# Performance work log

Measured on AMD Instinct MI355X. Metric: run time of the kernel, lower is better.

## Reference

```python
import jax, jax.numpy as jnp
import numpy as np

B, T = 2, 512
D, H, DFF = 1024, 16, 4096
V, CSL = 32000, 16
NL, NDL = 4, 2
MAXLEN = 1024
DH = D // H


def generate_ar_mask(L, csl):
    m = np.zeros((2 * L, 2 * L), dtype=bool)
    for i in range(L):
        m[:i] = True
        m[L + (i // csl) * csl: L + i] = True
    return jnp.asarray(m)


def generate_block_ntp_mask(L, csl):
    m = np.zeros((2 * L, 2 * L), dtype=bool)
    for c in range(L // csl):
        if c - 1 >= 0:
            m[:(c - 1) * csl] = True
        m[L + c * csl: L + (c + 1) * csl] = True
    return jnp.asarray(m)


def layernorm(x, g, b, eps=1e-5):
    mu = x.mean(-1, keepdims=True)
    var = x.var(-1, keepdims=True)
    return (x - mu) / jnp.sqrt(var + eps) * g + b


def block(x, mask, p):
    ln1g, ln1b, wqkv, bqkv, wo, bo, ln2g, ln2b, w1, b1, w2, b2 = p
    h = layernorm(x, ln1g, ln1b)
    qkv = h @ wqkv + bqkv                       # [B,S,3D]
    q, k, v = jnp.split(qkv, 3, axis=-1)
    bs, S, _ = x.shape
    q = q.reshape(bs, S, H, DH).transpose(0, 2, 1, 3)
    k = k.reshape(bs, S, H, DH).transpose(0, 2, 1, 3)
    v = v.reshape(bs, S, H, DH).transpose(0, 2, 1, 3)
    scores = jnp.einsum('bhqd,bhkd->bhqk', q, k) / jnp.sqrt(jnp.asarray(DH, x.dtype))
    scores = jnp.where(mask, scores, jnp.asarray(-1e9, x.dtype))
    attn = jax.nn.softmax(scores, axis=-1)
    o = jnp.einsum('bhqk,bhkd->bhqd', attn, v)
    o = o.transpose(0, 2, 1, 3).reshape(bs, S, D)
    x = x + (o @ wo + bo)
    h = layernorm(x, ln2g, ln2b)
    return x + (jax.nn.gelu(h @ w1 + b1, approximate=False) @ w2 + b2)


def setup_inputs():
    key = jax.random.key(0)
    ks = jax.random.split(key, 6)

    def pstack(k, n):
        kk = jax.random.split(k, 4)
        return dict(
            ln1g=jnp.ones((n, D)), ln1b=jnp.zeros((n, D)),
            wqkv=0.02 * jax.random.normal(kk[0], (n, D, 3 * D)), bqkv=jnp.zeros((n, 3 * D)),
            wo=0.02 * jax.random.normal(kk[1], (n, D, D)), bo=jnp.zeros((n, D)),
            ln2g=jnp.ones((n, D)), ln2b=jnp.zeros((n, D)),
            w1=0.02 * jax.random.normal(kk[2], (n, D, DFF)), b1=jnp.zeros((n, DFF)),
            w2=0.02 * jax.random.normal(kk[3], (n, DFF, D)), b2=jnp.zeros((n, D)))

    body = pstack(ks[0], NL)
    dec = pstack(ks[1], NDL)
    inp = {
        'tok_ids': jax.random.randint(ks[2], (B, T), 0, V),
        'tok_emb': 0.02 * jax.random.normal(ks[3], (V, D)),
        'pos_emb': 0.02 * jax.random.normal(ks[4], (MAXLEN, D)),
        'mask_tokens': 0.02 * jax.random.normal(ks[5], (1, CSL, D)),
    }
    for kname, vv in body.items():
        inp['b_' + kname] = vv
    for kname, vv in dec.items():
        inp['d_' + kname] = vv
    return inp


def reference(tok_ids, tok_emb, pos_emb, mask_tokens,
              b_ln1g, b_ln1b, b_wqkv, b_bqkv, b_wo, b_bo, b_ln2g, b_ln2b, b_w1, b_b1, b_w2, b_b2,
              d_ln1g, d_ln1b, d_wqkv, d_bqkv, d_wo, d_bo, d_ln2g, d_ln2b, d_w1, d_b1, d_w2, d_b2):
    Bq, Tq = tok_ids.shape
    pos = jnp.tile(jnp.arange(Tq), 2)            # pos ids repeated for both halves
    emb_pos = pos_emb[pos]                       # [2T, D], broadcast over batch
    mask_ids = jnp.tile(mask_tokens, (Bq, Tq // CSL, 1))
    x = jnp.concatenate([tok_emb[tok_ids], mask_ids], axis=1) + emb_pos[None]

    body_mask = generate_block_ntp_mask(Tq, CSL)
    bp = (b_ln1g, b_ln1b, b_wqkv, b_bqkv, b_wo, b_bo, b_ln2g, b_ln2b, b_w1, b_b1, b_w2, b_b2)
    for i in range(NL):
        x = block(x, body_mask, tuple(p[i] for p in bp))

    ar_mask = generate_ar_mask(Tq, CSL)
    dp = (d_ln1g, d_ln1b, d_wqkv, d_bqkv, d_wo, d_bo, d_ln2g, d_ln2b, d_w1, d_b1, d_w2, d_b2)
    for i in range(NDL):
        x = block(x, ar_mask, tuple(p[i] for p in dp))

    logits = (x @ tok_emb.T)[:, Tq + 1:, :]      # [B, T-1, V]
    tgt = tok_ids[:, :-1].reshape(-1)
    logits = logits.reshape(-1, V)
    logp = jax.nn.log_softmax(logits, axis=-1)
    loss = -jnp.take_along_axis(logp, tgt[:, None], axis=1).mean()
    return loss
```

## Files before the change

### kernel.cpp

```cpp
#include <hip/hip_runtime.h>
#include <hip/hip_bf16.h>
#include <math.h>

#define DD   1024
#define HHN  16
#define DHD  64
#define DFFN 4096
#define VV   32000
#define BBN  2
#define TTN  512
#define SSN  1024
#define NRN  2048

typedef __attribute__((ext_vector_type(8))) short short8;
typedef __attribute__((ext_vector_type(4))) float f32x4;

enum : long {
    LSTR    = 12582912,
    OFF_QKV = 0,
    OFF_WO  = 3145728,
    OFF_W1  = 4194304,
    OFF_W2  = 8388608
};

struct P24 { const float* p[24]; };

__device__ __forceinline__ unsigned short f2bf(float f) {
    __hip_bfloat16 h = __float2bfloat16(f);
    return __builtin_bit_cast(unsigned short, h);
}
__device__ __forceinline__ float bf2f(unsigned short u) {
    return __bfloat162float(__builtin_bit_cast(__hip_bfloat16, u));
}

__device__ __forceinline__ void glds16(const void* g, void* l) {
    __builtin_amdgcn_global_load_lds(
        (const __attribute__((address_space(1))) void*)g,
        (__attribute__((address_space(3))) void*)l,
        16, 0, 0);
}

__device__ __forceinline__ float blockReduceSum(float v) {
    __shared__ float sh[4];
    #pragma unroll
    for (int o = 1; o < 64; o <<= 1) v += __shfl_xor(v, o, 64);
    int lane = threadIdx.x & 63, wv = threadIdx.x >> 6;
    __syncthreads();
    if (lane == 0) sh[wv] = v;
    __syncthreads();
    return sh[0] + sh[1] + sh[2] + sh[3];
}

__global__ __launch_bounds__(256) void prep_k(P24 wp, unsigned short* __restrict__ wbf,
                                              const int* __restrict__ tok,
                                              const float* __restrict__ temb,
                                              const float* __restrict__ pemb,
                                              const float* __restrict__ mtok,
                                              float* __restrict__ x) {
    __shared__ __align__(16) unsigned short Lb[128 * 72];
    const int id = blockIdx.x;
    const int t = threadIdx.x;

    if (id < 9216) {
        int seg, base, K, N;
        long woff;
        if (id < 2304)      { seg = 0; base = 0;    K = DD;   N = 3 * DD; woff = OFF_QKV; }
        else if (id < 3072) { seg = 1; base = 2304; K = DD;   N = DD;     woff = OFF_WO;  }
        else if (id < 6144) { seg = 2; base = 3072; K = DD;   N = DFFN;   woff = OFF_W1;  }
        else                { seg = 3; base = 6144; K = DFFN; N = DD;     woff = OFF_W2;  }
        const int rid = id - base;
        const int tpl = (K / 128) * (N / 64);
        const int lz = rid / tpl, t2 = rid % tpl;
        const int nt = N / 64;
        const int n0 = (t2 % nt) * 64, k0 = (t2 / nt) * 128;
        const float* w = wp.p[seg * 6 + lz];
        unsigned short* wt = wbf + (size_t)lz * LSTR + woff;

        const int kr = t >> 4;
        const int nc = (t & 15) * 4;
        #pragma unroll
        for (int p = 0; p < 8; p++) {
            const int k = p * 16 + kr;
            const int g = ((k >> 6) & 1) << 4;
            float4 f = *(const float4*)(w + (size_t)(k0 + k) * N + n0 + nc);
            __align__(8) unsigned short tmp[4];
            tmp[0] = f2bf(f.x); tmp[1] = f2bf(f.y);
            tmp[2] = f2bf(f.z); tmp[3] = f2bf(f.w);
            *(unsigned long long*)&Lb[k * 72 + (nc ^ g)] =
                *(const unsigned long long*)tmp;
        }
        __syncthreads();
        {
            const int rp  = t >> 3;
            const int sub = t & 7;
            const int kcg = sub >> 2;
            const int kh  = sub & 3;
            const int colx = (2 * rp) ^ (kcg << 4);
            const int kb = kcg * 64 + kh * 16;
            __align__(16) unsigned short tA[16], tB[16];
            #pragma unroll
            for (int i = 0; i < 16; i++) {
                unsigned int v = *(const unsigned int*)&Lb[(kb + i) * 72 + colx];
                tA[i] = (unsigned short)(v & 0xffff);
                tB[i] = (unsigned short)(v >> 16);
            }
            unsigned short* d0 = wt + (size_t)(n0 + 2 * rp) * K + k0 + kb;
            unsigned short* d1 = d0 + K;
            #pragma unroll
            for (int i = 0; i < 2; i++) {
                ((int4*)d0)[i] = ((const int4*)tA)[i];
                ((int4*)d1)[i] = ((const int4*)tB)[i];
            }
        }
    } else {
        const int row = id - 9216;
        const int b = row >> 10, s = row & 1023;
        const int d = t * 4;
        const float* src;
        const float* pe;
        if (s < TTN) {
            int tid2 = tok[b * TTN + s];
            src = temb + (size_t)tid2 * DD + d;
            pe  = pemb + (size_t)s * DD + d;
        } else {
            int sm = s - TTN;
            src = mtok + (size_t)(sm & 15) * DD + d;
            pe  = pemb + (size_t)sm * DD + d;
        }
        float4 v = *(const float4*)src;
        float4 p = *(const float4*)pe;
        v.x += p.x; v.y += p.y; v.z += p.z; v.w += p.w;
        *(float4*)(x + (size_t)row * DD + d) = v;
    }
}

__global__ __launch_bounds__(256) void ln_k(const float* __restrict__ x,
                                            const float* __restrict__ g,
                                            const float* __restrict__ b,
                                            unsigned short* __restrict__ out) {
    int row = blockIdx.x;
    int d = threadIdx.x * 4;
    const float4 v = *(const float4*)(x + (size_t)row * DD + d);
    float s  = v.x + v.y + v.z + v.w;
    float ss = v.x * v.x + v.y * v.y + v.z * v.z + v.w * v.w;
    s  = blockReduceSum(s);
    ss = blockReduceSum(ss);
    float mu  = s * (1.0f / DD);
    float var = ss * (1.0f / DD) - mu * mu;
    float inv = rsqrtf(var + 1e-5f);
    const float4 gg = *(const float4*)(g + d);
    const float4 bb = *(const float4*)(b + d);
    ushort4 o;
    o.x = f2bf((v.x - mu) * inv * gg.x + bb.x);
    o.y = f2bf((v.y - mu) * inv * gg.y + bb.y);
    o.z = f2bf((v.z - mu) * inv * gg.z + bb.z);
    o.w = f2bf((v.w - mu) * inv * gg.w + bb.w);
    *(ushort4*)(out + (size_t)row * DD + d) = o;
}

__global__ __launch_bounds__(256, 4) void flash_k(
    const unsigned short* __restrict__ qkvb,
    unsigned short* __restrict__ o,
    int mtype) {
    __shared__ __align__(16) unsigned short Qs[64][72];
    __shared__ __align__(16) unsigned short Ks[64][72];
    __shared__ __align__(16) unsigned short Vs[64][72];
    __shared__ __align__(16) unsigned short Ps[64][72];
    __shared__ float vcol[64];

    const int blk = blockIdx.x;
    const int bh = blk >> 4, qt = blk & 15;
    const int b = bh >> 4, h = bh & 15;
    const int t = threadIdx.x;
    const int lane = t & 63;
    const int w = t >> 6;
    const int fr = lane & 15;
    const int g8 = (lane >> 4) * 8;
    const int g4 = (lane >> 4) * 4;

    {
        const int r = t >> 2, c0 = (t & 3) * 16;
        const unsigned short* src =
            qkvb + (size_t)(b * SSN + qt * 64 + r) * 3072 + h * 64 + c0;
        *(int4*)&Qs[r][c0]     = *(const int4*)(src);
        *(int4*)&Qs[r][c0 + 8] = *(const int4*)(src + 8);
    }
    __syncthreads();
    short8 aq[2];
    #pragma unroll
    for (int kk = 0; kk < 2; kk++)
        aq[kk] = *(const short8*)&Qs[w * 16 + fr][kk * 32 + g8];

    float rsum[4] = {0.f, 0.f, 0.f, 0.f};
    f32x4 accO[4] = {};

    float vacc[16];
    #pragma unroll
    for (int j = 0; j < 16; j++) vacc[j] = 0.f;

    const unsigned short* kbase = qkvb + (size_t)(b * SSN) * 3072 + DD + h * 64;
    const unsigned short* vbase = qkvb + (size_t)(b * SSN) * 3072 + 2 * DD + h * 64;
    const int d0 = w * 16;

    for (int kt = 0; kt < 16; kt++) {
        __syncthreads();
        {
            const int r = t >> 2, c0 = (t & 3) * 16;
            const unsigned short* src = kbase + (size_t)(kt * 64 + r) * 3072 + c0;
            *(int4*)&Ks[r][c0]     = *(const int4*)(src);
            *(int4*)&Ks[r][c0 + 8] = *(const int4*)(src + 8);
        }
        {
            const unsigned short* src = vbase + (size_t)(kt * 64 + lane) * 3072 + d0;
            int4 q0 = *(const int4*)(src);
            int4 q1 = *(const int4*)(src + 8);
            const unsigned short* u = (const unsigned short*)&q0;
            #pragma unroll
            for (int j = 0; j < 8; j++) {
                Vs[d0 + j][lane] = u[j];
                vacc[j] += bf2f(u[j]);
            }
            const unsigned short* u2 = (const unsigned short*)&q1;
            #pragma unroll
            for (int j = 0; j < 8; j++) {
                Vs[d0 + 8 + j][lane] = u2[j];
                vacc[8 + j] += bf2f(u2[j]);
            }
        }
        __syncthreads();

        f32x4 a2[4] = {};
        #pragma unroll
        for (int n = 0; n < 4; n++) {
            short8 bk0 = *(const short8*)&Ks[n * 16 + fr][g8];
            short8 bk1 = *(const short8*)&Ks[n * 16 + fr][32 + g8];
            a2[n] = __builtin_amdgcn_mfma_f32_16x16x32_bf16(aq[0], bk0, a2[n], 0, 0, 0);
            a2[n] = __builtin_amdgcn_mfma_f32_16x16x32_bf16(aq[1], bk1, a2[n], 0, 0, 0);
        }
        #pragma unroll
        for (int j = 0; j < 4; j++) {
            #pragma unroll
            for (int n = 0; n < 4; n++) {
                float pv = __expf(a2[n][j] * 0.125f);
                rsum[j] += pv;
                Ps[w * 16 + g4 + j][n * 16 + fr] = f2bf(pv);
            }
        }
        #pragma unroll
        for (int kk = 0; kk < 2; kk++) {
            short8 pa = *(const short8*)&Ps[w * 16 + fr][kk * 32 + g8];
            #pragma unroll
            for (int nd = 0; nd < 4; nd++) {
                short8 vb = *(const short8*)&Vs[nd * 16 + fr][kk * 32 + g8];
                accO[nd] = __builtin_amdgcn_mfma_f32_16x16x32_bf16(pa, vb, accO[nd], 0, 0, 0);
            }
        }
    }

    float lrun[4];
    #pragma unroll
    for (int j = 0; j < 4; j++) {
        float rs = rsum[j];
        #pragma unroll
        for (int o2 = 1; o2 < 16; o2 <<= 1) rs += __shfl_xor(rs, o2, 64);
        lrun[j] = rs;
    }

    #pragma unroll
    for (int j = 0; j < 16; j++) {
        float vs = vacc[j];
        #pragma unroll
        for (int o2 = 1; o2 < 64; o2 <<= 1) vs += __shfl_xor(vs, o2, 64);
        if (lane == j) vcol[d0 + j] = vs;
    }
    __syncthreads();

    #pragma unroll
    for (int nd = 0; nd < 4; nd++)
        #pragma unroll
        for (int j = 0; j < 4; j++) {
            const int row = qt * 64 + w * 16 + g4 + j;
            const int col = nd * 16 + fr;
            bool uni;
            if (mtype == 0) uni = (row >= 480 && row < 512);
            else            uni = (row == 511) || (row >= 512 && (row & 15) == 15);
            float val;
            if (uni) val = vcol[col] * (1.0f / 1024.0f);
            else     val = accO[nd][j] / lrun[j];
            o[(size_t)(b * SSN + row) * DD + h * 64 + col] = f2bf(val);
        }
}

__global__ __launch_bounds__(256) void gxlconv_k(const float* __restrict__ x,
                                                 unsigned short* __restrict__ xl,
                                                 const float* __restrict__ temb,
                                                 unsigned short* __restrict__ tembb) {
    const int id = blockIdx.x;
    const int t = threadIdx.x;
    if (id < 1024) {
        int d = t * 4;
        ushort4 o = {0, 0, 0, 0};
        if (id < 1022) {
            int b = id / 511, i = id % 511;
            float4 v = *(const float4*)(x + (size_t)(b * SSN + 513 + i) * DD + d);
            o.x = f2bf(v.x); o.y = f2bf(v.y); o.z = f2bf(v.z); o.w = f2bf(v.w);
        }
        *(ushort4*)(xl + (size_t)id * DD + d) = o;
    } else {
        long i = ((long)(id - 1024) * 256 + t) * 8;
        float4 a = *(const float4*)(temb + i);
        float4 b = *(const float4*)(temb + i + 4);
        __align__(16) unsigned short tmp[8];
        tmp[0] = f2bf(a.x); tmp[1] = f2bf(a.y); tmp[2] = f2bf(a.z); tmp[3] = f2bf(a.w);
        tmp[4] = f2bf(b.x); tmp[5] = f2bf(b.y); tmp[6] = f2bf(b.z); tmp[7] = f2bf(b.w);
        *(int4*)(tembb + i) = *(const int4*)tmp;
    }
}

__global__ __launch_bounds__(256) void loss_row2_k(const float2* __restrict__ part,
                                                   const float* __restrict__ tgtlog,
                                                   float* __restrict__ rowloss) {
    const int r = blockIdx.x;
    const int t = threadIdx.x;
    float mx = -1e30f, s = 0.f;
    for (int i = t; i < 500; i += 256) {
        float2 p = part[(size_t)r * 500 + i];
        float m2 = fmaxf(mx, p.x);
        s = s * __expf(mx - m2) + p.y * __expf(p.x - m2);
        mx = m2;
    }
    #pragma unroll
    for (int o2 = 1; o2 < 64; o2 <<= 1) {
        float om = __shfl_xor(mx, o2, 64);
        float os = __shfl_xor(s, o2, 64);
        float m2 = fmaxf(mx, om);
        s = s * __expf(mx - m2) + os * __expf(om - m2);
        mx = m2;
    }
    __shared__ float shm[4], shs[4];
    int lane = t & 63, wv = t >> 6;
    if (lane == 0) { shm[wv] = mx; shs[wv] = s; }
    __syncthreads();
    if (t == 0) {
        float M = fmaxf(fmaxf(shm[0], shm[1]), fmaxf(shm[2], shm[3]));
        float S = shs[0] * __expf(shm[0] - M) + shs[1] * __expf(shm[1] - M)
                + shs[2] * __expf(shm[2] - M) + shs[3] * __expf(shm[3] - M);
        rowloss[r] = (logf(S) + M) - tgtlog[r];
    }
}

__global__ __launch_bounds__(256) void loss_final_k(const float* __restrict__ rowloss,
                                                    float* __restrict__ out) {
    int t = threadIdx.x;
    float s = 0.f;
    for (int i = t; i < 1022; i += 256) s += rowloss[i];
    s = blockReduceSum(s);
    if (t == 0) out[0] = s * (1.0f / 1022.0f);
}

template <int EPI, int KSPLIT, int BM>
__global__ __launch_bounds__(256) void gemm_k(
    const unsigned short* __restrict__ A, long lda,
    const unsigned short* __restrict__ Bt, long ldb,
    void* __restrict__ Cp, long ldc,
    const float* __restrict__ bias,
    int MT, int K, long kstr) {
    constexpr int MFRAG = BM / 32;
    __shared__ __align__(16) unsigned short As[2][BM][32];
    __shared__ __align__(16) unsigned short Bs[2][128][32];

    const int nwg = gridDim.x;
    const int q = nwg >> 3, r = nwg & 7;
    const int xcd = blockIdx.x & 7, lin = blockIdx.x >> 3;
    const int wg = (xcd < r ? xcd * (q + 1) : r * (q + 1) + (xcd - r) * q) + lin;
    const int tiles = nwg / KSPLIT;
    const int ks = wg / tiles;
    const int rem = wg % tiles;
    const int brow = (rem % MT) * BM;
    const int bcol = (rem / MT) * 128;
    const int Kl = K / KSPLIT;

    const int t = threadIdx.x;
    const int lane = t & 63;
    const int w = t >> 6;
    const int fr = lane & 15;
    const int g8 = (lane >> 4) * 8;

    const int sc = (lane & 3) * 8;
    const int srB = w * 32 + (lane >> 2);
    const unsigned short* bP0 = Bt + (size_t)(bcol + srB) * ldb + ks * Kl + sc;
    const unsigned short* bP1 = bP0 + (size_t)16 * ldb;
    const int srA = (BM == 128 ? w * 32 : w * 16) + (lane >> 2);
    const unsigned short* aP0 = A + (size_t)(brow + srA) * lda + ks * Kl + sc;
    const unsigned short* aP1 = aP0 + (size_t)16 * lda;

    f32x4 acc[MFRAG][4] = {};
    const int nsteps = Kl >> 5;

    auto stage = [&](int buf) {
        if constexpr (BM == 128) {
            glds16(aP0, &As[buf][w * 32][0]);
            glds16(aP1, &As[buf][w * 32 + 16][0]);
        } else {
            glds16(aP0, &As[buf][w * 16][0]);
        }
        glds16(bP0, &Bs[buf][w * 32][0]);
        glds16(bP1, &Bs[buf][w * 32 + 16][0]);
        aP0 += 32; aP1 += 32; bP0 += 32; bP1 += 32;
    };

    stage(0);
    asm volatile("s_waitcnt vmcnt(0)");
    __syncthreads();

    const int wrB = (w >> 1) * (BM / 2);
    int cur = 0;
    for (int s2 = 1; s2 < nsteps; ++s2) {
        const int nb = cur ^ 1;
        stage(nb);

        short8 af[MFRAG], bf[4];
        #pragma unroll
        for (int m = 0; m < MFRAG; m++)
            af[m] = *(const short8*)&As[cur][wrB + m * 16 + fr][g8];
        #pragma unroll
        for (int n = 0; n < 4; n++)
            bf[n] = *(const short8*)&Bs[cur][(w & 1) * 64 + n * 16 + fr][g8];
        #pragma unroll
        for (int m = 0; m < MFRAG; m++)
            #pragma unroll
            for (int n = 0; n < 4; n++)
                acc[m][n] = __builtin_amdgcn_mfma_f32_16x16x32_bf16(af[m], bf[n], acc[m][n], 0, 0, 0);
        __syncthreads();
        cur = nb;
    }
    {
        short8 af[MFRAG], bf[4];
        #pragma unroll
        for (int m = 0; m < MFRAG; m++)
            af[m] = *(const short8*)&As[cur][wrB + m * 16 + fr][g8];
        #pragma unroll
        for (int n = 0; n < 4; n++)
            bf[n] = *(const short8*)&Bs[cur][(w & 1) * 64 + n * 16 + fr][g8];
        #pragma unroll
        for (int m = 0; m < MFRAG; m++)
            #pragma unroll
            for (int n = 0; n < 4; n++)
                acc[m][n] = __builtin_amdgcn_mfma_f32_16x16x32_bf16(af[m], bf[n], acc[m][n], 0, 0, 0);
    }

    const int wc = (w & 1) * 64;
    const int g4 = (lane >> 4) * 4;
    #pragma unroll
    for (int n = 0; n < 4; n++) {
        const int col = bcol + wc + n * 16 + fr;
        const float bv = (bias && (KSPLIT == 1 || ks == 0)) ? bias[col] : 0.f;
        #pragma unroll
        for (int m = 0; m < MFRAG; m++) {
            #pragma unroll
            for (int j = 0; j < 4; j++) {
                const int row = brow + wrB + m * 16 + g4 + j;
                float v = acc[m][n][j] + bv;
                const size_t ci = (size_t)row * ldc + col;
                if (EPI == 0) {
                    ((float*)Cp)[ci] = v;
                } else if (EPI == 1) {
                    ((unsigned short*)Cp)[ci] = f2bf(v);
                } else if (EPI == 2) {
                    float gl = 0.5f * v * (1.0f + erff(v * 0.70710678118654752f));
                    ((unsigned short*)Cp)[ci] = f2bf(gl);
                } else if (EPI == 3) {
                    ((float*)Cp)[ci] += v;
                } else {
                    atomicAdd(&((float*)Cp)[ci], v);
                }
            }
        }
    }
}

__global__ __launch_bounds__(256) void gemm_lse_k(
    const unsigned short* __restrict__ A,
    const unsigned short* __restrict__ Bt,
    float2* __restrict__ part,
    float* __restrict__ tgtlog,
    const int* __restrict__ tok) {
    __shared__ __align__(16) unsigned short As[2][128][32];
    __shared__ __align__(16) unsigned short Bs[2][128][32];

    const int nwg = gridDim.x;
    const int q = nwg >> 3, r = nwg & 7;
    const int xcd = blockIdx.x & 7, lin = blockIdx.x >> 3;
    const int wg = (xcd < r ? xcd * (q + 1) : r * (q + 1) + (xcd - r) * q) + lin;
    const int MT = 8;
    const int brow = (wg % MT) * 128;
    const int bcol = (wg / MT) * 128;

    const int t = threadIdx.x;
    const int lane = t & 63;
    const int w = t >> 6;
    const int fr = lane & 15;
    const int g8 = (lane >> 4) * 8;

    const int sr = w * 32 + (lane >> 2);
    const int sc = (lane & 3) * 8;
    const unsigned short* aP0 = A + (size_t)(brow + sr) * DD + sc;
    const unsigned short* aP1 = aP0 + (size_t)16 * DD;
    const unsigned short* bP0 = Bt + (size_t)(bcol + sr) * DD + sc;
    const unsigned short* bP1 = bP0 + (size_t)16 * DD;

    f32x4 acc[4][4] = {};

    glds16(aP0, &As[0][w * 32][0]);
    glds16(aP1, &As[0][w * 32 + 16][0]);
    glds16(bP0, &Bs[0][w * 32][0]);
    glds16(bP1, &Bs[0][w * 32 + 16][0]);
    aP0 += 32; aP1 += 32; bP0 += 32; bP1 += 32;
    asm volatile("s_waitcnt vmcnt(0)");
    __syncthreads();

    int cur = 0;
    for (int s2 = 1; s2 < 32; ++s2) {
        const int nb = cur ^ 1;
        glds16(aP0, &As[nb][w * 32][0]);
        glds16(aP1, &As[nb][w * 32 + 16][0]);
        glds16(bP0, &Bs[nb][w * 32][0]);
        glds16(bP1, &Bs[nb][w * 32 + 16][0]);
        aP0 += 32; aP1 += 32; bP0 += 32; bP1 += 32;

        short8 af[4], bf[4];
        #pragma unroll
        for (int m = 0; m < 4; m++)
            af[m] = *(const short8*)&As[cur][(w >> 1) * 64 + m * 16 + fr][g8];
        #pragma unroll
        for (int n = 0; n < 4; n++)
            bf[n] = *(const short8*)&Bs[cur][(w & 1) * 64 + n * 16 + fr][g8];
        #pragma unroll
        for (int m = 0; m < 4; m++)
            #pragma unroll
            for (int n = 0; n < 4; n++)
                acc[m][n] = __builtin_amdgcn_mfma_f32_16x16x32_bf16(af[m], bf[n], acc[m][n], 0, 0, 0);
        __syncthreads();
        cur = nb;
    }
    {
        short8 af[4], bf[4];
        #pragma unroll
        for (int m = 0; m < 4; m++)
            af[m] = *(const short8*)&As[cur][(w >> 1) * 64 + m * 16 + fr][g8];
        #pragma unroll
        for (int n = 0; n < 4; n++)
            bf[n] = *(const short8*)&Bs[cur][(w & 1) * 64 + n * 16 + fr][g8];
        #pragma unroll
        for (int m = 0; m < 4; m++)
            #pragma unroll
            for (int n = 0; n < 4; n++)
                acc[m][n] = __builtin_amdgcn_mfma_f32_16x16x32_bf16(af[m], bf[n], acc[m][n], 0, 0, 0);
    }

    const int wr = (w >> 1) * 64;
    const int wc = (w & 1) * 64;
    const int g4 = (lane >> 4) * 4;
    const int ct2 = (bcol >> 7) * 2 + (w & 1);
    #pragma unroll
    for (int m = 0; m < 4; m++) {
        #pragma unroll
        for (int j = 0; j < 4; j++) {
            const int grow = brow + wr + m * 16 + g4 + j;
            const float v0 = acc[m][0][j], v1 = acc[m][1][j];
            const float v2 = acc[m][2][j], v3 = acc[m][3][j];
            float mx = fmaxf(fmaxf(v0, v1), fmaxf(v2, v3));
            #pragma unroll
            for (int o2 = 1; o2 < 16; o2 <<= 1) mx = fmaxf(mx, __shfl_xor(mx, o2, 64));
            float s = __expf(v0 - mx) + __expf(v1 - mx) + __expf(v2 - mx) + __expf(v3 - mx);
            #pragma unroll
            for (int o2 = 1; o2 < 16; o2 <<= 1) s += __shfl_xor(s, o2, 64);
            if (fr == 0) {
                float2 p; p.x = mx; p.y = s;
                part[(size_t)grow * 500 + ct2] = p;
            }
            int tgtc = -1;
            if (grow < 511) tgtc = tok[grow];
            else if (grow >= 511 && grow < 1022) tgtc = tok[512 + grow - 511];
            const int cl = tgtc - (bcol + wc);
            if (tgtc >= 0 && cl >= 0 && cl < 64 && (cl & 15) == fr) {
                const float vv[4] = {v0, v1, v2, v3};
                tgtlog[grow] = vv[cl >> 4];
            }
        }
    }
}

extern "C" void kernel_launch(void* const* d_in, const int* in_sizes, int n_in,
                              void* d_out, int out_size, void* d_ws, size_t ws_size,
                              hipStream_t stream) {
    const int*   tok  = (const int*)d_in[0];
    const float* temb = (const float*)d_in[1];
    const float* pemb = (const float*)d_in[2];
    const float* mtok = (const float*)d_in[3];
    const float* W[24];
    for (int i = 0; i < 24; i++) W[i] = (const float*)d_in[4 + i];

    char* ws = (char*)d_ws;
    float*          x      = (float*)(ws + 0);
    unsigned short* xb     = (unsigned short*)(ws + 8388608);
    unsigned short* qkvb   = (unsigned short*)(ws + 12582912);
    unsigned short* o      = (unsigned short*)(ws + 25165824);
    unsigned short* g      = (unsigned short*)(ws + 29360128);
    unsigned short* wbf    = (unsigned short*)(ws + 79691776);
    unsigned short* tembb  = (unsigned short*)(ws + 79691776);
    float2*         part   = (float2*)(ws + 145227776);
    float*          tgtlog = (float*)(ws + 149327872);
    unsigned short* xl     = (unsigned short*)(ws + 230686720);
    float*          rowloss= (float*)(ws + 232783872);

    P24 wp;
    for (int l = 0; l < 6; l++) {
        const int grp = (l < 4) ? 0 : 1;
        const int li  = (l < 4) ? l : l - 4;
        const float* const* P = W + grp * 12;
        wp.p[0 + l]  = P[2]  + (size_t)li * DD * 3 * DD;
        wp.p[6 + l]  = P[4]  + (size_t)li * DD * DD;
        wp.p[12 + l] = P[8]  + (size_t)li * DD * DFFN;
        wp.p[18 + l] = P[10] + (size_t)li * DFFN * DD;
    }
    prep_k<<<9216 + 2048, 256, 0, stream>>>(wp, wbf, tok, temb, pemb, mtok, x);

    for (int l = 0; l < 6; l++) {
        const int grp = (l < 4) ? 0 : 1;
        const int li  = (l < 4) ? l : l - 4;
        const float* const* P = W + grp * 12;
        const float* ln1g = P[0] + (size_t)li * DD;
        const float* ln1b = P[1] + (size_t)li * DD;
        const float* bqkv = P[3] + (size_t)li * 3 * DD;
        const float* bo   = P[5] + (size_t)li * DD;
        const float* ln2g = P[6] + (size_t)li * DD;
        const float* ln2b = P[7] + (size_t)li * DD;
        const float* b1   = P[9] + (size_t)li * DFFN;
        const float* b2   = P[11] + (size_t)li * DD;
        unsigned short* wl = wbf + (size_t)l * LSTR;

        if (l == 0) ln_k<<<NRN, 256, 0, stream>>>(x, ln1g, ln1b, xb);
        gemm_k<1, 1, 64><<<32 * 24, 256, 0, stream>>>(xb, DD, wl + OFF_QKV, DD,
                                                      qkvb, 3 * DD, bqkv, 32, DD, 0);
        flash_k<<<512, 256, 0, stream>>>(qkvb, o, grp);
        gemm_k<3, 1, 64><<<32 * 8, 256, 0, stream>>>(o, DD, wl + OFF_WO, DD,
                                                     x, DD, bo, 32, DD, 0);

        ln_k<<<NRN, 256, 0, stream>>>(x, ln2g, ln2b, xb);
        gemm_k<2, 1, 128><<<16 * 32, 256, 0, stream>>>(xb, DD, wl + OFF_W1, DD,
                                                       g, DFFN, b1, 16, DD, 0);
        gemm_k<4, 4, 128><<<16 * 8 * 4, 256, 0, stream>>>(g, DFFN, wl + OFF_W2, DFFN,
                                                          x, DD, b2, 16, DFFN, 0);
        if (l < 5) {
            const int l2 = l + 1;
            const int grp2 = (l2 < 4) ? 0 : 1;
            const int li2  = (l2 < 4) ? l2 : l2 - 4;
            const float* const* P2 = W + grp2 * 12;
            ln_k<<<NRN, 256, 0, stream>>>(x, P2[0] + (size_t)li2 * DD,
                                          P2[1] + (size_t)li2 * DD, xb);
        } else {
            gxlconv_k<<<1024 + 16000, 256, 0, stream>>>(x, xl, temb, tembb);
        }
    }

    gemm_lse_k<<<2000, 256, 0, stream>>>(xl, tembb, part, tgtlog, tok);
    loss_row2_k<<<1022, 256, 0, stream>>>(part, tgtlog, rowloss);
    loss_final_k<<<1, 256, 0, stream>>>(rowloss, (float*)d_out);
}
```

Measured before the change: 1.404 ms.

## Fuse all transformer layers into persistent megakernel with grid barriers

Replaces the per-layer chain of LN, GEMM and flash-attention launches with one persistent kernel of 512 blocks. The blocks step through every stage and synchronise with a software grid barrier built on atomics. The tok_emb bf16 conversion moves into the prep kernel, and the final loss reduction is folded into the row kernel with an atomic add. This removes about 40 launches and their tail gaps. In exchange, every stage now runs with fixed tile shapes, and correctness depends on all 512 blocks being co-resident (launch bounds of 2 blocks per CU); otherwise the barrier can deadlock.

```diff
diff --git a/kernel.cpp b/kernel.cpp
--- a/kernel.cpp
+++ b/kernel.cpp
@@ -24,6 +24,10 @@
 };
 
 struct P24 { const float* p[24]; };
+struct MegaP {
+    const float *ln1g[6], *ln1b[6], *bqkv[6], *bo[6];
+    const float *ln2g[6], *ln2b[6], *b1[6], *b2[6];
+};
 
 __device__ __forceinline__ unsigned short f2bf(float f) {
     __hip_bfloat16 h = __float2bfloat16(f);
@@ -40,15 +44,18 @@
         16, 0, 0);
 }
 
-__device__ __forceinline__ float blockReduceSum(float v) {
-    __shared__ float sh[4];
-    #pragma unroll
-    for (int o = 1; o < 64; o <<= 1) v += __shfl_xor(v, o, 64);
-    int lane = threadIdx.x & 63, wv = threadIdx.x >> 6;
-    __syncthreads();
-    if (lane == 0) sh[wv] = v;
-    __syncthreads();
-    return sh[0] + sh[1] + sh[2] + sh[3];
+__device__ __forceinline__ void gbar(unsigned* bar, unsigned nb) {
+    __syncthreads();
+    if (threadIdx.x == 0) {
+        __threadfence();
+        unsigned old = __hip_atomic_fetch_add(bar, 1u, __ATOMIC_RELEASE,
+                                              __HIP_MEMORY_SCOPE_AGENT);
+        const unsigned need = (old / nb + 1u) * nb;
+        while (__hip_atomic_load(bar, __ATOMIC_ACQUIRE,
+                                 __HIP_MEMORY_SCOPE_AGENT) < need)
+            __builtin_amdgcn_s_sleep(8);
+    }
+    __syncthreads();
 }
 
 __global__ __launch_bounds__(256) void prep_k(P24 wp, unsigned short* __restrict__ wbf,
@@ -56,7 +63,8 @@
                                               const float* __restrict__ temb,
                                               const float* __restrict__ pemb,
                                               const float* __restrict__ mtok,
-                                              float* __restrict__ x) {
+                                              float* __restrict__ x,
+                                              unsigned short* __restrict__ tembb) {
     __shared__ __align__(16) unsigned short Lb[128 * 72];
     const int id = blockIdx.x;
     const int t = threadIdx.x;
@@ -112,7 +120,7 @@
                 ((int4*)d1)[i] = ((const int4*)tB)[i];
             }
         }
-    } else {
+    } else if (id < 11264) {
         const int row = id - 9216;
         const int b = row >> 10, s = row & 1023;
         const int d = t * 4;
@@ -131,43 +139,169 @@
         float4 p = *(const float4*)pe;
         v.x += p.x; v.y += p.y; v.z += p.z; v.w += p.w;
         *(float4*)(x + (size_t)row * DD + d) = v;
-    }
-}
-
-__global__ __launch_bounds__(256) void ln_k(const float* __restrict__ x,
+    } else {
+        long i = ((long)(id - 11264) * 256 + t) * 8;
+        float4 a = *(const float4*)(temb + i);
+        float4 b = *(const float4*)(temb + i + 4);
+        __align__(16) unsigned short tmp[8];
+        tmp[0] = f2bf(a.x); tmp[1] = f2bf(a.y); tmp[2] = f2bf(a.z); tmp[3] = f2bf(a.w);
+        tmp[4] = f2bf(b.x); tmp[5] = f2bf(b.y); tmp[6] = f2bf(b.z); tmp[7] = f2bf(b.w);
+        *(int4*)(tembb + i) = *(const int4*)tmp;
+    }
+}
+
+
+__device__ __forceinline__ void dev_ln_wave(const float* __restrict__ x,
                                             const float* __restrict__ g,
                                             const float* __restrict__ b,
-                                            unsigned short* __restrict__ out) {
-    int row = blockIdx.x;
-    int d = threadIdx.x * 4;
-    const float4 v = *(const float4*)(x + (size_t)row * DD + d);
-    float s  = v.x + v.y + v.z + v.w;
-    float ss = v.x * v.x + v.y * v.y + v.z * v.z + v.w * v.w;
-    s  = blockReduceSum(s);
-    ss = blockReduceSum(ss);
-    float mu  = s * (1.0f / DD);
-    float var = ss * (1.0f / DD) - mu * mu;
-    float inv = rsqrtf(var + 1e-5f);
-    const float4 gg = *(const float4*)(g + d);
-    const float4 bb = *(const float4*)(b + d);
-    ushort4 o;
-    o.x = f2bf((v.x - mu) * inv * gg.x + bb.x);
-    o.y = f2bf((v.y - mu) * inv * gg.y + bb.y);
-    o.z = f2bf((v.z - mu) * inv * gg.z + bb.z);
-    o.w = f2bf((v.w - mu) * inv * gg.w + bb.w);
-    *(ushort4*)(out + (size_t)row * DD + d) = o;
-}
-
-__global__ __launch_bounds__(256, 4) void flash_k(
-    const unsigned short* __restrict__ qkvb,
-    unsigned short* __restrict__ o,
-    int mtype) {
-    __shared__ __align__(16) unsigned short Qs[64][72];
-    __shared__ __align__(16) unsigned short Ks[64][72];
-    __shared__ __align__(16) unsigned short Vs[64][72];
-    __shared__ __align__(16) unsigned short Ps[64][72];
-    __shared__ float vcol[64];
-
+                                            unsigned short* __restrict__ out, int row) {
+    const int lane = threadIdx.x & 63;
+    float4 v[4];
+    float s = 0.f, ss = 0.f;
+    #pragma unroll
+    for (int c = 0; c < 4; c++) {
+        v[c] = *(const float4*)(x + (size_t)row * DD + c * 256 + lane * 4);
+        s  += v[c].x + v[c].y + v[c].z + v[c].w;
+        ss += v[c].x * v[c].x + v[c].y * v[c].y + v[c].z * v[c].z + v[c].w * v[c].w;
+    }
+    #pragma unroll
+    for (int o2 = 1; o2 < 64; o2 <<= 1) {
+        s  += __shfl_xor(s, o2, 64);
+        ss += __shfl_xor(ss, o2, 64);
+    }
+    const float mu  = s * (1.0f / DD);
+    const float var = ss * (1.0f / DD) - mu * mu;
+    const float inv = rsqrtf(var + 1e-5f);
+    #pragma unroll
+    for (int c = 0; c < 4; c++) {
+        const int d = c * 256 + lane * 4;
+        const float4 gg = *(const float4*)(g + d);
+        const float4 bb = *(const float4*)(b + d);
+        ushort4 ov;
+        ov.x = f2bf((v[c].x - mu) * inv * gg.x + bb.x);
+        ov.y = f2bf((v[c].y - mu) * inv * gg.y + bb.y);
+        ov.z = f2bf((v[c].z - mu) * inv * gg.z + bb.z);
+        ov.w = f2bf((v[c].w - mu) * inv * gg.w + bb.w);
+        *(ushort4*)(out + (size_t)row * DD + d) = ov;
+    }
+}
+
+template <int EPI, int BM>
+__device__ __forceinline__ void dev_gemm(
+    unsigned short* LDSU,
+    int brow, int bcol, long kOff, int Kl, bool addBias,
+    const unsigned short* __restrict__ A, long lda,
+    const unsigned short* __restrict__ Bt, long ldb,
+    void* __restrict__ Cp, long ldc,
+    const float* __restrict__ bias) {
+    constexpr int MFRAG = BM / 32;
+    unsigned short* AsB = LDSU;
+    unsigned short* BsB = LDSU + 2 * BM * 32;
+
+    const int t = threadIdx.x;
+    const int lane = t & 63;
+    const int w = t >> 6;
+    const int fr = lane & 15;
+    const int g8 = (lane >> 4) * 8;
+
+    const int sc = (lane & 3) * 8;
+    const int srB = w * 32 + (lane >> 2);
+    const unsigned short* bP0 = Bt + (size_t)(bcol + srB) * ldb + kOff + sc;
+    const unsigned short* bP1 = bP0 + (size_t)16 * ldb;
+    const int srA = (BM == 128 ? w * 32 : w * 16) + (lane >> 2);
+    const unsigned short* aP0 = A + (size_t)(brow + srA) * lda + kOff + sc;
+    const unsigned short* aP1 = aP0 + (size_t)16 * lda;
+
+    f32x4 acc[MFRAG][4] = {};
+    const int nsteps = Kl >> 5;
+
+    auto stage = [&](int buf) {
+        unsigned short* ab = AsB + buf * (BM * 32);
+        unsigned short* bb = BsB + buf * (128 * 32);
+        if constexpr (BM == 128) {
+            glds16(aP0, ab + (w * 32) * 32);
+            glds16(aP1, ab + (w * 32 + 16) * 32);
+        } else {
+            glds16(aP0, ab + (w * 16) * 32);
+        }
+        glds16(bP0, bb + (w * 32) * 32);
+        glds16(bP1, bb + (w * 32 + 16) * 32);
+        aP0 += 32; aP1 += 32; bP0 += 32; bP1 += 32;
+    };
+
+    stage(0);
+    asm volatile("s_waitcnt vmcnt(0)");
+    __syncthreads();
+
+    const int wrB = (w >> 1) * (BM / 2);
+    int cur = 0;
+    for (int s2 = 1; s2 < nsteps; ++s2) {
+        const int nb = cur ^ 1;
+        stage(nb);
+
+        short8 af[MFRAG], bf[4];
+        #pragma unroll
+        for (int m = 0; m < MFRAG; m++)
+            af[m] = *(const short8*)(AsB + cur * (BM * 32) + (wrB + m * 16 + fr) * 32 + g8);
+        #pragma unroll
+        for (int n = 0; n < 4; n++)
+            bf[n] = *(const short8*)(BsB + cur * (128 * 32) + ((w & 1) * 64 + n * 16 + fr) * 32 + g8);
+        #pragma unroll
+        for (int m = 0; m < MFRAG; m++)
+            #pragma unroll
+            for (int n = 0; n < 4; n++)
+                acc[m][n] = __builtin_amdgcn_mfma_f32_16x16x32_bf16(af[m], bf[n], acc[m][n], 0, 0, 0);
+        __syncthreads();
+        cur = nb;
+    }
+    {
+        short8 af[MFRAG], bf[4];
+        #pragma unroll
+        for (int m = 0; m < MFRAG; m++)
+            af[m] = *(const short8*)(AsB + cur * (BM * 32) + (wrB + m * 16 + fr) * 32 + g8);
+        #pragma unroll
+        for (int n = 0; n < 4; n++)
+            bf[n] = *(const short8*)(BsB + cur * (128 * 32) + ((w & 1) * 64 + n * 16 + fr) * 32 + g8);
+        #pragma unroll
+        for (int m = 0; m < MFRAG; m++)
+            #pragma unroll
+            for (int n = 0; n < 4; n++)
+                acc[m][n] = __builtin_amdgcn_mfma_f32_16x16x32_bf16(af[m], bf[n], acc[m][n], 0, 0, 0);
+    }
+    __syncthreads();
+
+    const int wc = (w & 1) * 64;
+    const int g4 = (lane >> 4) * 4;
+    #pragma unroll
+    for (int n = 0; n < 4; n++) {
+        const int col = bcol + wc + n * 16 + fr;
+        const float bv = (bias && addBias) ? bias[col] : 0.f;
+        #pragma unroll
+        for (int m = 0; m < MFRAG; m++) {
+            #pragma unroll
+            for (int j = 0; j < 4; j++) {
+                const int row = brow + wrB + m * 16 + g4 + j;
+                float v = acc[m][n][j] + bv;
+                const size_t ci = (size_t)row * ldc + col;
+                if (EPI == 1) {
+                    ((unsigned short*)Cp)[ci] = f2bf(v);
+                } else if (EPI == 2) {
+                    float gl = 0.5f * v * (1.0f + erff(v * 0.70710678118654752f));
+                    ((unsigned short*)Cp)[ci] = f2bf(gl);
+                } else if (EPI == 3) {
+                    ((float*)Cp)[ci] += v;
+                } else {
+                    atomicAdd(&((float*)Cp)[ci], v);
+                }
+            }
+        }
+    }
+}
+
+__device__ __forceinline__ void dev_flash(unsigned short* Lf,
+                                          const unsigned short* __restrict__ qkvb,
+                                          unsigned short* __restrict__ o, int mtype) {
+    float* vcol = (float*)(Lf + 18432);
     const int blk = blockIdx.x;
     const int bh = blk >> 4, qt = blk & 15;
     const int b = bh >> 4, h = bh & 15;
@@ -182,18 +316,17 @@
         const int r = t >> 2, c0 = (t & 3) * 16;
         const unsigned short* src =
             qkvb + (size_t)(b * SSN + qt * 64 + r) * 3072 + h * 64 + c0;
-        *(int4*)&Qs[r][c0]     = *(const int4*)(src);
-        *(int4*)&Qs[r][c0 + 8] = *(const int4*)(src + 8);
+        *(int4*)&Lf[r * 72 + c0]     = *(const int4*)(src);
+        *(int4*)&Lf[r * 72 + c0 + 8] = *(const int4*)(src + 8);
     }
     __syncthreads();
     short8 aq[2];
     #pragma unroll
     for (int kk = 0; kk < 2; kk++)
-        aq[kk] = *(const short8*)&Qs[w * 16 + fr][kk * 32 + g8];
+        aq[kk] = *(const short8*)&Lf[(w * 16 + fr) * 72 + kk * 32 + g8];
 
     float rsum[4] = {0.f, 0.f, 0.f, 0.f};
     f32x4 accO[4] = {};
-
     float vacc[16];
     #pragma unroll
     for (int j = 0; j < 16; j++) vacc[j] = 0.f;
@@ -207,8 +340,8 @@
         {
             const int r = t >> 2, c0 = (t & 3) * 16;
             const unsigned short* src = kbase + (size_t)(kt * 64 + r) * 3072 + c0;
-            *(int4*)&Ks[r][c0]     = *(const int4*)(src);
-            *(int4*)&Ks[r][c0 + 8] = *(const int4*)(src + 8);
+            *(int4*)&Lf[4608 + r * 72 + c0]     = *(const int4*)(src);
+            *(int4*)&Lf[4608 + r * 72 + c0 + 8] = *(const int4*)(src + 8);
         }
         {
             const unsigned short* src = vbase + (size_t)(kt * 64 + lane) * 3072 + d0;
@@ -217,13 +350,13 @@
             const unsigned short* u = (const unsigned short*)&q0;
             #pragma unroll
             for (int j = 0; j < 8; j++) {
-                Vs[d0 + j][lane] = u[j];
+                Lf[9216 + (d0 + j) * 72 + lane] = u[j];
                 vacc[j] += bf2f(u[j]);
             }
             const unsigned short* u2 = (const unsigned short*)&q1;
             #pragma unroll
             for (int j = 0; j < 8; j++) {
-                Vs[d0 + 8 + j][lane] = u2[j];
+                Lf[9216 + (d0 + 8 + j) * 72 + lane] = u2[j];
                 vacc[8 + j] += bf2f(u2[j]);
             }
         }
@@ -232,8 +365,8 @@
         f32x4 a2[4] = {};
         #pragma unroll
         for (int n = 0; n < 4; n++) {
-            short8 bk0 = *(const short8*)&Ks[n * 16 + fr][g8];
-            short8 bk1 = *(const short8*)&Ks[n * 16 + fr][32 + g8];
+            short8 bk0 = *(const short8*)&Lf[4608 + (n * 16 + fr) * 72 + g8];
+            short8 bk1 = *(const short8*)&Lf[4608 + (n * 16 + fr) * 72 + 32 + g8];
             a2[n] = __builtin_amdgcn_mfma_f32_16x16x32_bf16(aq[0], bk0, a2[n], 0, 0, 0);
             a2[n] = __builtin_amdgcn_mfma_f32_16x16x32_bf16(aq[1], bk1, a2[n], 0, 0, 0);
         }
@@ -243,15 +376,15 @@
             for (int n = 0; n < 4; n++) {
                 float pv = __expf(a2[n][j] * 0.125f);
                 rsum[j] += pv;
-                Ps[w * 16 + g4 + j][n * 16 + fr] = f2bf(pv);
+                Lf[13824 + (w * 16 + g4 + j) * 72 + n * 16 + fr] = f2bf(pv);
             }
         }
         #pragma unroll
         for (int kk = 0; kk < 2; kk++) {
-            short8 pa = *(const short8*)&Ps[w * 16 + fr][kk * 32 + g8];
+            short8 pa = *(const short8*)&Lf[13824 + (w * 16 + fr) * 72 + kk * 32 + g8];
             #pragma unroll
             for (int nd = 0; nd < 4; nd++) {
-                short8 vb = *(const short8*)&Vs[nd * 16 + fr][kk * 32 + g8];
+                short8 vb = *(const short8*)&Lf[9216 + (nd * 16 + fr) * 72 + kk * 32 + g8];
                 accO[nd] = __builtin_amdgcn_mfma_f32_16x16x32_bf16(pa, vb, accO[nd], 0, 0, 0);
             }
         }
@@ -265,7 +398,6 @@
         for (int o2 = 1; o2 < 16; o2 <<= 1) rs += __shfl_xor(rs, o2, 64);
         lrun[j] = rs;
     }
-
     #pragma unroll
     for (int j = 0; j < 16; j++) {
         float vs = vacc[j];
@@ -289,37 +421,191 @@
             else     val = accO[nd][j] / lrun[j];
             o[(size_t)(b * SSN + row) * DD + h * 64 + col] = f2bf(val);
         }
-}
-
-__global__ __launch_bounds__(256) void gxlconv_k(const float* __restrict__ x,
-                                                 unsigned short* __restrict__ xl,
-                                                 const float* __restrict__ temb,
-                                                 unsigned short* __restrict__ tembb) {
-    const int id = blockIdx.x;
+    __syncthreads();
+}
+
+__device__ __forceinline__ void dev_gxl(const float* __restrict__ x,
+                                        unsigned short* __restrict__ xl, int r) {
+    const int d = threadIdx.x * 4;
+    ushort4 ov = {0, 0, 0, 0};
+    if (r < 1022) {
+        int b = r / 511, i = r % 511;
+        float4 v = *(const float4*)(x + (size_t)(b * SSN + 513 + i) * DD + d);
+        ov.x = f2bf(v.x); ov.y = f2bf(v.y); ov.z = f2bf(v.z); ov.w = f2bf(v.w);
+    }
+    if (r < 1024) *(ushort4*)(xl + (size_t)r * DD + d) = ov;
+}
+
+__global__ __launch_bounds__(256, 2) void mega_k(
+    MegaP P, const unsigned short* __restrict__ wbf,
+    float* __restrict__ x, unsigned short* __restrict__ xb,
+    unsigned short* __restrict__ qkvb, unsigned short* __restrict__ o,
+    unsigned short* __restrict__ g, unsigned short* __restrict__ xl,
+    unsigned* bar) {
+    __shared__ __align__(16) unsigned short LDSU[18560];
+    const int blk = blockIdx.x;
+    const unsigned NB = gridDim.x;
+
+    dev_ln_wave(x, P.ln1g[0], P.ln1b[0], xb, blk * 4 + (threadIdx.x >> 6));
+    gbar(bar, NB);
+
+    for (int l = 0; l < 6; ++l) {
+        const unsigned short* wl = wbf + (size_t)l * LSTR;
+
+        for (int tt = blk; tt < 384; tt += NB)
+            dev_gemm<1, 128>(LDSU, (tt & 15) * 128, (tt >> 4) * 128, 0, DD, true,
+                             xb, DD, wl + OFF_QKV, DD, qkvb, 3 * DD, P.bqkv[l]);
+        gbar(bar, NB);
+
+        dev_flash(LDSU, qkvb, o, (l < 4) ? 0 : 1);
+        gbar(bar, NB);
+
+        for (int tt = blk; tt < 256; tt += NB)
+            dev_gemm<3, 64>(LDSU, (tt & 31) * 64, (tt >> 5) * 128, 0, DD, true,
+                            o, DD, wl + OFF_WO, DD, x, DD, P.bo[l]);
+        gbar(bar, NB);
+
+        dev_ln_wave(x, P.ln2g[l], P.ln2b[l], xb, blk * 4 + (threadIdx.x >> 6));
+        gbar(bar, NB);
+
+        for (int tt = blk; tt < 512; tt += NB)
+            dev_gemm<2, 128>(LDSU, (tt & 15) * 128, (tt >> 4) * 128, 0, DD, true,
+                             xb, DD, wl + OFF_W1, DD, g, DFFN, P.b1[l]);
+        gbar(bar, NB);
+
+        for (int tt = blk; tt < 512; tt += NB) {
+            const int rem = tt & 127, ks = tt >> 7;
+            dev_gemm<4, 128>(LDSU, (rem & 15) * 128, (rem >> 4) * 128,
+                             (long)ks * 1024, 1024, ks == 0,
+                             g, DFFN, wl + OFF_W2, DFFN, x, DD, P.b2[l]);
+        }
+        gbar(bar, NB);
+
+        if (l < 5) {
+            dev_ln_wave(x, P.ln1g[l + 1], P.ln1b[l + 1], xb, blk * 4 + (threadIdx.x >> 6));
+            gbar(bar, NB);
+        } else {
+            dev_gxl(x, xl, blk * 2);
+            dev_gxl(x, xl, blk * 2 + 1);
+        }
+    }
+}
+
+__global__ __launch_bounds__(256) void gemm_lse_k(
+    const unsigned short* __restrict__ A,
+    const unsigned short* __restrict__ Bt,
+    float2* __restrict__ part,
+    float* __restrict__ tgtlog,
+    const int* __restrict__ tok) {
+    __shared__ __align__(16) unsigned short As[2][128][32];
+    __shared__ __align__(16) unsigned short Bs[2][128][32];
+
+    const int nwg = gridDim.x;
+    const int q = nwg >> 3, r = nwg & 7;
+    const int xcd = blockIdx.x & 7, lin = blockIdx.x >> 3;
+    const int wg = (xcd < r ? xcd * (q + 1) : r * (q + 1) + (xcd - r) * q) + lin;
+    const int MT = 8;
+    const int brow = (wg % MT) * 128;
+    const int bcol = (wg / MT) * 128;
+
     const int t = threadIdx.x;
-    if (id < 1024) {
-        int d = t * 4;
-        ushort4 o = {0, 0, 0, 0};
-        if (id < 1022) {
-            int b = id / 511, i = id % 511;
-            float4 v = *(const float4*)(x + (size_t)(b * SSN + 513 + i) * DD + d);
-            o.x = f2bf(v.x); o.y = f2bf(v.y); o.z = f2bf(v.z); o.w = f2bf(v.w);
-        }
-        *(ushort4*)(xl + (size_t)id * DD + d) = o;
-    } else {
-        long i = ((long)(id - 1024) * 256 + t) * 8;
-        float4 a = *(const float4*)(temb + i);
-        float4 b = *(const float4*)(temb + i + 4);
-        __align__(16) unsigned short tmp[8];
-        tmp[0] = f2bf(a.x); tmp[1] = f2bf(a.y); tmp[2] = f2bf(a.z); tmp[3] = f2bf(a.w);
-        tmp[4] = f2bf(b.x); tmp[5] = f2bf(b.y); tmp[6] = f2bf(b.z); tmp[7] = f2bf(b.w);
-        *(int4*)(tembb + i) = *(const int4*)tmp;
+    const int lane = t & 63;
+    const int w = t >> 6;
+    const int fr = lane & 15;
+    const int g8 = (lane >> 4) * 8;
+
+    const int sr = w * 32 + (lane >> 2);
+    const int sc = (lane & 3) * 8;
+    const unsigned short* aP0 = A + (size_t)(brow + sr) * DD + sc;
+    const unsigned short* aP1 = aP0 + (size_t)16 * DD;
+    const unsigned short* bP0 = Bt + (size_t)(bcol + sr) * DD + sc;
+    const unsigned short* bP1 = bP0 + (size_t)16 * DD;
+
+    f32x4 acc[4][4] = {};
+
+    glds16(aP0, &As[0][w * 32][0]);
+    glds16(aP1, &As[0][w * 32 + 16][0]);
+    glds16(bP0, &Bs[0][w * 32][0]);
+    glds16(bP1, &Bs[0][w * 32 + 16][0]);
+    aP0 += 32; aP1 += 32; bP0 += 32; bP1 += 32;
+    asm volatile("s_waitcnt vmcnt(0)");
+    __syncthreads();
+
+    int cur = 0;
+    for (int s2 = 1; s2 < 32; ++s2) {
+        const int nb = cur ^ 1;
+        glds16(aP0, &As[nb][w * 32][0]);
+        glds16(aP1, &As[nb][w * 32 + 16][0]);
+        glds16(bP0, &Bs[nb][w * 32][0]);
+        glds16(bP1, &Bs[nb][w * 32 + 16][0]);
+        aP0 += 32; aP1 += 32; bP0 += 32; bP1 += 32;
+
+        short8 af[4], bf[4];
+        #pragma unroll
+        for (int m = 0; m < 4; m++)
+            af[m] = *(const short8*)&As[cur][(w >> 1) * 64 + m * 16 + fr][g8];
+        #pragma unroll
+        for (int n = 0; n < 4; n++)
+            bf[n] = *(const short8*)&Bs[cur][(w & 1) * 64 + n * 16 + fr][g8];
+        #pragma unroll
+        for (int m = 0; m < 4; m++)
+            #pragma unroll
+            for (int n = 0; n < 4; n++)
+                acc[m][n] = __builtin_amdgcn_mfma_f32_16x16x32_bf16(af[m], bf[n], acc[m][n], 0, 0, 0);
+        __syncthreads();
+        cur = nb;
+    }
+    {
+        short8 af[4], bf[4];
+        #pragma unroll
+        for (int m = 0; m < 4; m++)
+            af[m] = *(const short8*)&As[cur][(w >> 1) * 64 + m * 16 + fr][g8];
+        #pragma unroll
+        for (int n = 0; n < 4; n++)
+            bf[n] = *(const short8*)&Bs[cur][(w & 1) * 64 + n * 16 + fr][g8];
+        #pragma unroll
+        for (int m = 0; m < 4; m++)
+            #pragma unroll
+            for (int n = 0; n < 4; n++)
+                acc[m][n] = __builtin_amdgcn_mfma_f32_16x16x32_bf16(af[m], bf[n], acc[m][n], 0, 0, 0);
+    }
+
+    const int wr = (w >> 1) * 64;
+    const int wc = (w & 1) * 64;
+    const int g4 = (lane >> 4) * 4;
+    const int ct2 = (bcol >> 7) * 2 + (w & 1);
+    #pragma unroll
+    for (int m = 0; m < 4; m++) {
+        #pragma unroll
+        for (int j = 0; j < 4; j++) {
+            const int grow = brow + wr + m * 16 + g4 + j;
+            const float v0 = acc[m][0][j], v1 = acc[m][1][j];
+            const float v2 = acc[m][2][j], v3 = acc[m][3][j];
+            float mx = fmaxf(fmaxf(v0, v1), fmaxf(v2, v3));
+            #pragma unroll
+            for (int o2 = 1; o2 < 16; o2 <<= 1) mx = fmaxf(mx, __shfl_xor(mx, o2, 64));
+            float s = __expf(v0 - mx) + __expf(v1 - mx) + __expf(v2 - mx) + __expf(v3 - mx);
+            #pragma unroll
+            for (int o2 = 1; o2 < 16; o2 <<= 1) s += __shfl_xor(s, o2, 64);
+            if (fr == 0) {
+                float2 p; p.x = mx; p.y = s;
+                part[(size_t)grow * 500 + ct2] = p;
+            }
+            int tgtc = -1;
+            if (grow < 511) tgtc = tok[grow];
+            else if (grow >= 511 && grow < 1022) tgtc = tok[512 + grow - 511];
+            const int cl = tgtc - (bcol + wc);
+            if (tgtc >= 0 && cl >= 0 && cl < 64 && (cl & 15) == fr) {
+                const float vv[4] = {v0, v1, v2, v3};
+                tgtlog[grow] = vv[cl >> 4];
+            }
+        }
     }
 }
 
 __global__ __launch_bounds__(256) void loss_row2_k(const float2* __restrict__ part,
                                                    const float* __restrict__ tgtlog,
-                                                   float* __restrict__ rowloss) {
+                                                   float* __restrict__ out) {
     const int r = blockIdx.x;
     const int t = threadIdx.x;
     float mx = -1e30f, s = 0.f;
@@ -345,249 +631,7 @@
         float M = fmaxf(fmaxf(shm[0], shm[1]), fmaxf(shm[2], shm[3]));
         float S = shs[0] * __expf(shm[0] - M) + shs[1] * __expf(shm[1] - M)
                 + shs[2] * __expf(shm[2] - M) + shs[3] * __expf(shm[3] - M);
-        rowloss[r] = (logf(S) + M) - tgtlog[r];
-    }
-}
-
-__global__ __launch_bounds__(256) void loss_final_k(const float* __restrict__ rowloss,
-                                                    float* __restrict__ out) {
-    int t = threadIdx.x;
-    float s = 0.f;
-    for (int i = t; i < 1022; i += 256) s += rowloss[i];
-    s = blockReduceSum(s);
-    if (t == 0) out[0] = s * (1.0f / 1022.0f);
-}
-
-template <int EPI, int KSPLIT, int BM>
-__global__ __launch_bounds__(256) void gemm_k(
-    const unsigned short* __restrict__ A, long lda,
-    const unsigned short* __restrict__ Bt, long ldb,
-    void* __restrict__ Cp, long ldc,
-    const float* __restrict__ bias,
-    int MT, int K, long kstr) {
-    constexpr int MFRAG = BM / 32;
-    __shared__ __align__(16) unsigned short As[2][BM][32];
-    __shared__ __align__(16) unsigned short Bs[2][128][32];
-
-    const int nwg = gridDim.x;
-    const int q = nwg >> 3, r = nwg & 7;
-    const int xcd = blockIdx.x & 7, lin = blockIdx.x >> 3;
-    const int wg = (xcd < r ? xcd * (q + 1) : r * (q + 1) + (xcd - r) * q) + lin;
-    const int tiles = nwg / KSPLIT;
-    const int ks = wg / tiles;
-    const int rem = wg % tiles;
-    const int brow = (rem % MT) * BM;
-    const int bcol = (rem / MT) * 128;
-    const int Kl = K / KSPLIT;
-
-    const int t = threadIdx.x;
-    const int lane = t & 63;
-    const int w = t >> 6;
-    const int fr = lane & 15;
-    const int g8 = (lane >> 4) * 8;
-
-    const int sc = (lane & 3) * 8;
-    const int srB = w * 32 + (lane >> 2);
-    const unsigned short* bP0 = Bt + (size_t)(bcol + srB) * ldb + ks * Kl + sc;
-    const unsigned short* bP1 = bP0 + (size_t)16 * ldb;
-    const int srA = (BM == 128 ? w * 32 : w * 16) + (lane >> 2);
-    const unsigned short* aP0 = A + (size_t)(brow + srA) * lda + ks * Kl + sc;
-    const unsigned short* aP1 = aP0 + (size_t)16 * lda;
-
-    f32x4 acc[MFRAG][4] = {};
-    const int nsteps = Kl >> 5;
-
-    auto stage = [&](int buf) {
-        if constexpr (BM == 128) {
-            glds16(aP0, &As[buf][w * 32][0]);
-            glds16(aP1, &As[buf][w * 32 + 16][0]);
-        } else {
-            glds16(aP0, &As[buf][w * 16][0]);
-        }
-        glds16(bP0, &Bs[buf][w * 32][0]);
-        glds16(bP1, &Bs[buf][w * 32 + 16][0]);
-        aP0 += 32; aP1 += 32; bP0 += 32; bP1 += 32;
-    };
-
-    stage(0);
-    asm volatile("s_waitcnt vmcnt(0)");
-    __syncthreads();
-
-    const int wrB = (w >> 1) * (BM / 2);
-    int cur = 0;
-    for (int s2 = 1; s2 < nsteps; ++s2) {
-        const int nb = cur ^ 1;
-        stage(nb);
-
-        short8 af[MFRAG], bf[4];
-        #pragma unroll
-        for (int m = 0; m < MFRAG; m++)
-            af[m] = *(const short8*)&As[cur][wrB + m * 16 + fr][g8];
-        #pragma unroll
-        for (int n = 0; n < 4; n++)
-            bf[n] = *(const short8*)&Bs[cur][(w & 1) * 64 + n * 16 + fr][g8];
-        #pragma unroll
-        for (int m = 0; m < MFRAG; m++)
-            #pragma unroll
-            for (int n = 0; n < 4; n++)
-                acc[m][n] = __builtin_amdgcn_mfma_f32_16x16x32_bf16(af[m], bf[n], acc[m][n], 0, 0, 0);
-        __syncthreads();
-        cur = nb;
-    }
-    {
-        short8 af[MFRAG], bf[4];
-        #pragma unroll
-        for (int m = 0; m < MFRAG; m++)
-            af[m] = *(const short8*)&As[cur][wrB + m * 16 + fr][g8];
-        #pragma unroll
-        for (int n = 0; n < 4; n++)
-            bf[n] = *(const short8*)&Bs[cur][(w & 1) * 64 + n * 16 + fr][g8];
-        #pragma unroll
-        for (int m = 0; m < MFRAG; m++)
-            #pragma unroll
-            for (int n = 0; n < 4; n++)
-                acc[m][n] = __builtin_amdgcn_mfma_f32_16x16x32_bf16(af[m], bf[n], acc[m][n], 0, 0, 0);
-    }
-
-    const int wc = (w & 1) * 64;
-    const int g4 = (lane >> 4) * 4;
-    #pragma unroll
-    for (int n = 0; n < 4; n++) {
-        const int col = bcol + wc + n * 16 + fr;
-        const float bv = (bias && (KSPLIT == 1 || ks == 0)) ? bias[col] : 0.f;
-        #pragma unroll
-        for (int m = 0; m < MFRAG; m++) {
-            #pragma unroll
-            for (int j = 0; j < 4; j++) {
-                const int row = brow + wrB + m * 16 + g4 + j;
-                float v = acc[m][n][j] + bv;
-                const size_t ci = (size_t)row * ldc + col;
-                if (EPI == 0) {
-                    ((float*)Cp)[ci] = v;
-                } else if (EPI == 1) {
-                    ((unsigned short*)Cp)[ci] = f2bf(v);
-                } else if (EPI == 2) {
-                    float gl = 0.5f * v * (1.0f + erff(v * 0.70710678118654752f));
-                    ((unsigned short*)Cp)[ci] = f2bf(gl);
-                } else if (EPI == 3) {
-                    ((float*)Cp)[ci] += v;
-                } else {
-                    atomicAdd(&((float*)Cp)[ci], v);
-                }
-            }
-        }
-    }
-}
-
-__global__ __launch_bounds__(256) void gemm_lse_k(
-    const unsigned short* __restrict__ A,
-    const unsigned short* __restrict__ Bt,
-    float2* __restrict__ part,
-    float* __restrict__ tgtlog,
-    const int* __restrict__ tok) {
-    __shared__ __align__(16) unsigned short As[2][128][32];
-    __shared__ __align__(16) unsigned short Bs[2][128][32];
-
-    const int nwg = gridDim.x;
-    const int q = nwg >> 3, r = nwg & 7;
-    const int xcd = blockIdx.x & 7, lin = blockIdx.x >> 3;
-    const int wg = (xcd < r ? xcd * (q + 1) : r * (q + 1) + (xcd - r) * q) + lin;
-    const int MT = 8;
-    const int brow = (wg % MT) * 128;
-    const int bcol = (wg / MT) * 128;
-
-    const int t = threadIdx.x;
-    const int lane = t & 63;
-    const int w = t >> 6;
-    const int fr = lane & 15;
-    const int g8 = (lane >> 4) * 8;
-
-    const int sr = w * 32 + (lane >> 2);
-    const int sc = (lane & 3) * 8;
-    const unsigned short* aP0 = A + (size_t)(brow + sr) * DD + sc;
-    const unsigned short* aP1 = aP0 + (size_t)16 * DD;
-    const unsigned short* bP0 = Bt + (size_t)(bcol + sr) * DD + sc;
-    const unsigned short* bP1 = bP0 + (size_t)16 * DD;
-
-    f32x4 acc[4][4] = {};
-
-    glds16(aP0, &As[0][w * 32][0]);
-    glds16(aP1, &As[0][w * 32 + 16][0]);
-    glds16(bP0, &Bs[0][w * 32][0]);
-    glds16(bP1, &Bs[0][w * 32 + 16][0]);
-    aP0 += 32; aP1 += 32; bP0 += 32; bP1 += 32;
-    asm volatile("s_waitcnt vmcnt(0)");
-    __syncthreads();
-
-    int cur = 0;
-    for (int s2 = 1; s2 < 32; ++s2) {
-        const int nb = cur ^ 1;
-        glds16(aP0, &As[nb][w * 32][0]);
-        glds16(aP1, &As[nb][w * 32 + 16][0]);
-        glds16(bP0, &Bs[nb][w * 32][0]);
-        glds16(bP1, &Bs[nb][w * 32 + 16][0]);
-        aP0 += 32; aP1 += 32; bP0 += 32; bP1 += 32;
-
-        short8 af[4], bf[4];
-        #pragma unroll
-        for (int m = 0; m < 4; m++)
-            af[m] = *(const short8*)&As[cur][(w >> 1) * 64 + m * 16 + fr][g8];
-        #pragma unroll
-        for (int n = 0; n < 4; n++)
-            bf[n] = *(const short8*)&Bs[cur][(w & 1) * 64 + n * 16 + fr][g8];
-        #pragma unroll
-        for (int m = 0; m < 4; m++)
-            #pragma unroll
-            for (int n = 0; n < 4; n++)
-                acc[m][n] = __builtin_amdgcn_mfma_f32_16x16x32_bf16(af[m], bf[n], acc[m][n], 0, 0, 0);
-        __syncthreads();
-        cur = nb;
-    }
-    {
-        short8 af[4], bf[4];
-        #pragma unroll
-        for (int m = 0; m < 4; m++)
-            af[m] = *(const short8*)&As[cur][(w >> 1) * 64 + m * 16 + fr][g8];
-        #pragma unroll
-        for (int n = 0; n < 4; n++)
-            bf[n] = *(const short8*)&Bs[cur][(w & 1) * 64 + n * 16 + fr][g8];
-        #pragma unroll
-        for (int m = 0; m < 4; m++)
-            #pragma unroll
-            for (int n = 0; n < 4; n++)
-                acc[m][n] = __builtin_amdgcn_mfma_f32_16x16x32_bf16(af[m], bf[n], acc[m][n], 0, 0, 0);
-    }
-
-    const int wr = (w >> 1) * 64;
-    const int wc = (w & 1) * 64;
-    const int g4 = (lane >> 4) * 4;
-    const int ct2 = (bcol >> 7) * 2 + (w & 1);
-    #pragma unroll
-    for (int m = 0; m < 4; m++) {
-        #pragma unroll
-        for (int j = 0; j < 4; j++) {
-            const int grow = brow + wr + m * 16 + g4 + j;
-            const float v0 = acc[m][0][j], v1 = acc[m][1][j];
-            const float v2 = acc[m][2][j], v3 = acc[m][3][j];
-            float mx = fmaxf(fmaxf(v0, v1), fmaxf(v2, v3));
-            #pragma unroll
-            for (int o2 = 1; o2 < 16; o2 <<= 1) mx = fmaxf(mx, __shfl_xor(mx, o2, 64));
-            float s = __expf(v0 - mx) + __expf(v1 - mx) + __expf(v2 - mx) + __expf(v3 - mx);
-            #pragma unroll
-            for (int o2 = 1; o2 < 16; o2 <<= 1) s += __shfl_xor(s, o2, 64);
-            if (fr == 0) {
-                float2 p; p.x = mx; p.y = s;
-                part[(size_t)grow * 500 + ct2] = p;
-            }
-            int tgtc = -1;
-            if (grow < 511) tgtc = tok[grow];
-            else if (grow >= 511 && grow < 1022) tgtc = tok[512 + grow - 511];
-            const int cl = tgtc - (bcol + wc);
-            if (tgtc >= 0 && cl >= 0 && cl < 64 && (cl & 15) == fr) {
-                const float vv[4] = {v0, v1, v2, v3};
-                tgtlog[grow] = vv[cl >> 4];
-            }
-        }
+        atomicAdd(out, ((logf(S) + M) - tgtlog[r]) * (1.0f / 1022.0f));
     }
 }
 
@@ -608,13 +652,15 @@
     unsigned short* o      = (unsigned short*)(ws + 25165824);
     unsigned short* g      = (unsigned short*)(ws + 29360128);
     unsigned short* wbf    = (unsigned short*)(ws + 79691776);
-    unsigned short* tembb  = (unsigned short*)(ws + 79691776);
-    float2*         part   = (float2*)(ws + 145227776);
-    float*          tgtlog = (float*)(ws + 149327872);
-    unsigned short* xl     = (unsigned short*)(ws + 230686720);
-    float*          rowloss= (float*)(ws + 232783872);
+    unsigned short* tembb  = (unsigned short*)(ws + 145227776);
+    tembb = (unsigned short*)(ws + 230686720);
+    float2*         part   = (float2*)(ws + 296222720);
+    float*          tgtlog = (float*)(ws + 300318720);
+    unsigned short* xl     = (unsigned short*)(ws + 300322816);
+    unsigned*       bar    = (unsigned*)(ws + 302419968);
 
     P24 wp;
+    MegaP mp;
     for (int l = 0; l < 6; l++) {
         const int grp = (l < 4) ? 0 : 1;
         const int li  = (l < 4) ? l : l - 4;
@@ -623,48 +669,21 @@
         wp.p[6 + l]  = P[4]  + (size_t)li * DD * DD;
         wp.p[12 + l] = P[8]  + (size_t)li * DD * DFFN;
         wp.p[18 + l] = P[10] + (size_t)li * DFFN * DD;
-    }
-    prep_k<<<9216 + 2048, 256, 0, stream>>>(wp, wbf, tok, temb, pemb, mtok, x);
-
-    for (int l = 0; l < 6; l++) {
-        const int grp = (l < 4) ? 0 : 1;
-        const int li  = (l < 4) ? l : l - 4;
-        const float* const* P = W + grp * 12;
-        const float* ln1g = P[0] + (size_t)li * DD;
-        const float* ln1b = P[1] + (size_t)li * DD;
-        const float* bqkv = P[3] + (size_t)li * 3 * DD;
-        const float* bo   = P[5] + (size_t)li * DD;
-        const float* ln2g = P[6] + (size_t)li * DD;
-        const float* ln2b = P[7] + (size_t)li * DD;
-        const float* b1   = P[9] + (size_t)li * DFFN;
-        const float* b2   = P[11] + (size_t)li * DD;
-        unsigned short* wl = wbf + (size_t)l * LSTR;
-
-        if (l == 0) ln_k<<<NRN, 256, 0, stream>>>(x, ln1g, ln1b, xb);
-        gemm_k<1, 1, 64><<<32 * 24, 256, 0, stream>>>(xb, DD, wl + OFF_QKV, DD,
-                                                      qkvb, 3 * DD, bqkv, 32, DD, 0);
-        flash_k<<<512, 256, 0, stream>>>(qkvb, o, grp);
-        gemm_k<3, 1, 64><<<32 * 8, 256, 0, stream>>>(o, DD, wl + OFF_WO, DD,
-                                                     x, DD, bo, 32, DD, 0);
-
-        ln_k<<<NRN, 256, 0, stream>>>(x, ln2g, ln2b, xb);
-        gemm_k<2, 1, 128><<<16 * 32, 256, 0, stream>>>(xb, DD, wl + OFF_W1, DD,
-                                                       g, DFFN, b1, 16, DD, 0);
-        gemm_k<4, 4, 128><<<16 * 8 * 4, 256, 0, stream>>>(g, DFFN, wl + OFF_W2, DFFN,
-                                                          x, DD, b2, 16, DFFN, 0);
-        if (l < 5) {
-            const int l2 = l + 1;
-            const int grp2 = (l2 < 4) ? 0 : 1;
-            const int li2  = (l2 < 4) ? l2 : l2 - 4;
-            const float* const* P2 = W + grp2 * 12;
-            ln_k<<<NRN, 256, 0, stream>>>(x, P2[0] + (size_t)li2 * DD,
-                                          P2[1] + (size_t)li2 * DD, xb);
-        } else {
-            gxlconv_k<<<1024 + 16000, 256, 0, stream>>>(x, xl, temb, tembb);
-        }
-    }
-
+        mp.ln1g[l] = P[0]  + (size_t)li * DD;
+        mp.ln1b[l] = P[1]  + (size_t)li * DD;
+        mp.bqkv[l] = P[3]  + (size_t)li * 3 * DD;
+        mp.bo[l]   = P[5]  + (size_t)li * DD;
+        mp.ln2g[l] = P[6]  + (size_t)li * DD;
+        mp.ln2b[l] = P[7]  + (size_t)li * DD;
+        mp.b1[l]   = P[9]  + (size_t)li * DFFN;
+        mp.b2[l]   = P[11] + (size_t)li * DD;
+    }
+
+    hipMemsetAsync(bar, 0, 256, stream);
+    hipMemsetAsync(d_out, 0, 4, stream);
+
+    prep_k<<<9216 + 2048 + 16000, 256, 0, stream>>>(wp, wbf, tok, temb, pemb, mtok, x, tembb);
+    mega_k<<<512, 256, 0, stream>>>(mp, wbf, x, xb, qkvb, o, g, xl, bar);
     gemm_lse_k<<<2000, 256, 0, stream>>>(xl, tembb, part, tgtlog, tok);
-    loss_row2_k<<<1022, 256, 0, stream>>>(part, tgtlog, rowloss);
-    loss_final_k<<<1, 256, 0, stream>>>(rowloss, (float*)d_out);
-}
+    loss_row2_k<<<1022, 256, 0, stream>>>(part, tgtlog, (float*)d_out);
+}
```

After: 4.498 ms. +220.4%, slower.
